# Kernel optimization log

Measured on AMD Instinct MI355X. Metric: run time of the kernel, lower is better.

The kernel has to match this reference:

```python
import jax, jax.numpy as jnp
import numpy as np

IOU_THRESHOLD = 0.5  # default in ObjectUtils.nms
N_BOXES = 10000


def setup_inputs() -> dict:
    key = jax.random.key(0)
    k1, k2 = jax.random.split(key)
    boxes = jax.random.uniform(k1, (N_BOXES, 4), dtype=jnp.float32)  # normalized cxcywh
    scores = jax.random.uniform(k2, (N_BOXES,), dtype=jnp.float32)
    return {"boxes_cxcywh": boxes, "scores": scores}


def _cxcywh_to_ltrb(b):
    cx, cy, w, h = b[:, 0], b[:, 1], b[:, 2], b[:, 3]
    return jnp.stack([cx - w / 2, cy - h / 2, cx + w / 2, cy + h / 2], axis=1)


def _pairwise_iou(a, b):
    # a: [N1,4] ltrb, b: [N2,4] ltrb -> [N1,N2] (matches ObjectUtils.compute_iou)
    lt = jnp.maximum(a[:, None, :2], b[None, :, :2])
    rb = jnp.minimum(a[:, None, 2:], b[None, :, 2:])
    wh = jnp.clip(rb - lt, 0.0)
    inter = wh[..., 0] * wh[..., 1]
    area_a = (a[:, 2] - a[:, 0]) * (a[:, 3] - a[:, 1])
    area_b = (b[:, 2] - b[:, 0]) * (b[:, 3] - b[:, 1])
    return inter / (area_a[:, None] + area_b[None, :] - inter)


def reference(boxes_cxcywh, scores):
    ltrb = _cxcywh_to_ltrb(boxes_cxcywh)
    iou = _pairwise_iou(ltrb, ltrb)  # [N,N]

    # ---- greedy NMS, faithful to ObjectUtils.nms (unclamped intersection,
    # retain when iou < threshold) expressed as a jit-friendly suppression loop ----
    n = ltrb.shape[0]
    order = jnp.argsort(-scores)  # highest score first (torch.sort ascending, pop last)
    bs = ltrb[order]
    l, t, r, b = bs[:, 0], bs[:, 1], bs[:, 2], bs[:, 3]
    area = (r - l) * (b - t)
    inter_nms = (jnp.minimum(r[:, None], r[None, :]) - jnp.maximum(l[:, None], l[None, :])) * \
                (jnp.minimum(b[:, None], b[None, :]) - jnp.maximum(t[:, None], t[None, :]))
    iou_nms = inter_nms / (area[:, None] + area[None, :] - inter_nms)
    ar = jnp.arange(n)

    def body(i, keep):
        # box i (in sorted order) suppresses lower-scored boxes only if it is itself kept
        suppress = keep[i] & (iou_nms[i] >= IOU_THRESHOLD) & (ar > i)
        return keep & jnp.logical_not(suppress)

    keep_sorted = jax.lax.fori_loop(0, n, body, jnp.ones((n,), dtype=bool))
    keep = jnp.zeros((n,), dtype=bool).at[order].set(keep_sorted)
    return iou, keep
```

## Files before the change

kernel.cpp:

```cpp
#include <hip/hip_runtime.h>

typedef unsigned long long u64;

#define THR 0.5f

__device__ __forceinline__ void conv_box(const float4 b, float& l, float& t,
                                         float& r, float& bo, float& a) {
  #pragma clang fp contract(off)
  float hw = 0.5f * b.z;
  float hh = 0.5f * b.w;
  l = b.x - hw;
  t = b.y - hh;
  r = b.x + hw;
  bo = b.y + hh;
  a = (r - l) * (bo - t);
}

__global__ void k_zero(int* __restrict__ rank, int n) {
  int i = blockIdx.x * blockDim.x + threadIdx.x;
  if (i < n) rank[i] = 0;
}

__global__ void k_rank(const float* __restrict__ scores, int* __restrict__ rank,
                       int n, int jchunk) {
  int i = blockIdx.x * blockDim.x + threadIdx.x;
  if (i >= n) return;
  float si = scores[i];
  int j0 = blockIdx.y * jchunk;
  int j1 = min(j0 + jchunk, n);
  int c = 0;
  for (int j = j0; j < j1; ++j) {
    float sj = scores[j];
    c += ((sj > si) || (sj == si && j < i)) ? 1 : 0;
  }
  if (c) atomicAdd(rank + i, c);
}

__global__ void k_scatter(const float4* __restrict__ boxes, const int* __restrict__ rank,
                          float* __restrict__ sl, float* __restrict__ st,
                          float* __restrict__ sr, float* __restrict__ sb,
                          float* __restrict__ sa, int* __restrict__ sidx, int n) {
  int i = blockIdx.x * blockDim.x + threadIdx.x;
  if (i >= n) return;
  float l, t, r, b, a;
  conv_box(boxes[i], l, t, r, b, a);
  int k = rank[i];
  sl[k] = l; st[k] = t; sr[k] = r; sb[k] = b; sa[k] = a; sidx[k] = i;
}

__device__ __forceinline__ void mask_body(
    const float* __restrict__ sl, const float* __restrict__ st,
    const float* __restrict__ sr, const float* __restrict__ sb,
    const float* __restrict__ sa,
    u64* __restrict__ mask, u64* __restrict__ diag, u64* __restrict__ band,
    int n, int wstride, int bx, int by) {
  #pragma clang fp contract(off)
  int k = bx * 256 + threadIdx.x;
  if (k >= n) return;
  int w = by;
  int jbase = w << 6;
  u64 word = 0;
  if (jbase + 63 > k) {
    float l = sl[k], t = st[k], r = sr[k], b = sb[k], a = sa[k];
    int jend = min(jbase + 64, n);
    for (int j = max(jbase, k + 1); j < jend; ++j) {
      float lmax = fmaxf(l, sl[j]);
      float tmax = fmaxf(t, st[j]);
      float rmin = fminf(r, sr[j]);
      float bmin = fminf(b, sb[j]);
      float wd = rmin - lmax;
      float hd = bmin - tmax;
      float inter = wd * hd;
      float denom = (a + sa[j]) - inter;
      float q = inter / denom;
      if (q >= THR) word |= 1ull << (j - jbase);
    }
  }
  mask[(size_t)k * wstride + w] = word;
  int kg = k >> 6;
  if (kg == w) diag[k] = word;
  if (w == kg + 1) band[k] = word;
}

__global__ void k_mask(const float* __restrict__ sl, const float* __restrict__ st,
                       const float* __restrict__ sr, const float* __restrict__ sb,
                       const float* __restrict__ sa,
                       u64* __restrict__ mask, u64* __restrict__ diag,
                       u64* __restrict__ band, int n, int wstride) {
  mask_body(sl, st, sr, sb, sa, mask, diag, band, n, wstride, blockIdx.x, blockIdx.y);
}

__device__ __forceinline__ u64 wave_or_u64(u64 v) {
  unsigned lo = (unsigned)v, hi = (unsigned)(v >> 32);
#define DPP_OR(x, ctrl, rmask) \
  x |= (unsigned)__builtin_amdgcn_update_dpp(0, (int)(x), ctrl, rmask, 0xF, true)
  DPP_OR(lo, 0x111, 0xF); DPP_OR(hi, 0x111, 0xF);
  DPP_OR(lo, 0x112, 0xF); DPP_OR(hi, 0x112, 0xF);
  DPP_OR(lo, 0x114, 0xF); DPP_OR(hi, 0x114, 0xF);
  DPP_OR(lo, 0x118, 0xF); DPP_OR(hi, 0x118, 0xF);
  DPP_OR(lo, 0x142, 0xA); DPP_OR(hi, 0x142, 0xA);
  DPP_OR(lo, 0x143, 0xC); DPP_OR(hi, 0x143, 0xC);
#undef DPP_OR
  unsigned flo = (unsigned)__builtin_amdgcn_readlane((int)lo, 63);
  unsigned fhi = (unsigned)__builtin_amdgcn_readlane((int)hi, 63);
  return ((u64)fhi << 32) | flo;
}

__device__ __forceinline__ void scan_body7(
    const u64* __restrict__ mask, const u64* __restrict__ diag,
    const u64* __restrict__ band, const int* __restrict__ sidx,
    float* __restrict__ keep, int n, int wstride,
    u64* rem, u64* dsh, u64* bsh, u64* kwords, int (*kept)[64], int* nk_sh) {
  int t = threadIdx.x, wv = t >> 6, lane = t & 63;
  int ng = (n + 63) >> 6;
  rem[t] = 0;
  if (t < 2) nk_sh[t] = 0;
  u64 bnd = 0;
  u64 x0 = 0, x1 = 0, x2 = 0, x3 = 0, x4 = 0, x5 = 0, x6 = 0, x7 = 0;
  const ulonglong2* d2 = (const ulonglong2*)dsh;
  if (wv == 0) {
    dsh[lane] = diag[lane];
    bsh[lane] = band[lane];
    ulonglong2 p0 = d2[0], p1 = d2[1], p2 = d2[2], p3 = d2[3];
    x0 = p0.x; x1 = p0.y; x2 = p1.x; x3 = p1.y;
    x4 = p2.x; x5 = p2.y; x6 = p3.x; x7 = p3.y;
  }
  __syncthreads();
  for (int g = 0; g < ng; ++g) {
    int base = g << 6;
    if (wv == 0) {
      int nxt = base + 64 + lane;
      u64 dnext = (g + 1 < ng) ? diag[nxt] : 0;
      u64 bnext = (g + 1 < ng) ? band[nxt] : 0;
      u64 bshv = bsh[lane];
      u64 s = rem[g] | bnd;
      int valid = n - base;
      if (valid < 64) s |= (~0ull) << valid;
      u64 kw = 0;
      u64 y0, y1, y2, y3, y4, y5, y6, y7;
#define LDC(a0,a1,a2,a3,a4,a5,a6,a7, c) { \
      ulonglong2 q0 = d2[4*(c)], q1 = d2[4*(c)+1], q2 = d2[4*(c)+2], q3 = d2[4*(c)+3]; \
      a0 = q0.x; a1 = q0.y; a2 = q1.x; a3 = q1.y; a4 = q2.x; a5 = q2.y; a6 = q3.x; a7 = q3.y; }
#define STEP(BB, EQ) if (!((s >> (BB)) & 1ull)) { kw |= 1ull << (BB); s |= EQ; }
#define CHUNK(b0v, a0,a1,a2,a3,a4,a5,a6,a7) \
      if ((unsigned)((s >> (b0v)) & 0xFFull) != 0xFFu) { \
        STEP(b0v+0, a0) STEP(b0v+1, a1) STEP(b0v+2, a2) STEP(b0v+3, a3) \
        STEP(b0v+4, a4) STEP(b0v+5, a5) STEP(b0v+6, a6) STEP(b0v+7, a7) }
      LDC(y0,y1,y2,y3,y4,y5,y6,y7, 1); CHUNK(0,  x0,x1,x2,x3,x4,x5,x6,x7);
      LDC(x0,x1,x2,x3,x4,x5,x6,x7, 2); CHUNK(8,  y0,y1,y2,y3,y4,y5,y6,y7);
      LDC(y0,y1,y2,y3,y4,y5,y6,y7, 3); CHUNK(16, x0,x1,x2,x3,x4,x5,x6,x7);
      LDC(x0,x1,x2,x3,x4,x5,x6,x7, 4); CHUNK(24, y0,y1,y2,y3,y4,y5,y6,y7);
      LDC(y0,y1,y2,y3,y4,y5,y6,y7, 5); CHUNK(32, x0,x1,x2,x3,x4,x5,x6,x7);
      LDC(x0,x1,x2,x3,x4,x5,x6,x7, 6); CHUNK(40, y0,y1,y2,y3,y4,y5,y6,y7);
      LDC(y0,y1,y2,y3,y4,y5,y6,y7, 7); CHUNK(48, x0,x1,x2,x3,x4,x5,x6,x7);
                                       CHUNK(56, y0,y1,y2,y3,y4,y5,y6,y7);
#undef CHUNK
#undef STEP
#undef LDC
      if (lane == 0) kwords[g] = kw;
      int nk = __popcll(kw);
      if ((kw >> lane) & 1ull) {
        int pos = __popcll(kw & ((1ull << lane) - 1ull));
        kept[g & 1][pos] = lane;
      }
      int npad = (nk + 15) & ~15;
      if (lane >= nk && lane < npad) kept[g & 1][lane] = 0;
      if (lane == 0) nk_sh[g & 1] = nk;
      u64 bv = ((kw >> lane) & 1ull) ? bshv : 0ull;
      bnd = wave_or_u64(bv);
      dsh[lane] = dnext;
      bsh[lane] = bnext;
      ulonglong2 p0 = d2[0], p1 = d2[1], p2 = d2[2], p3 = d2[3];
      x0 = p0.x; x1 = p0.y; x2 = p1.x; x3 = p1.y;
      x4 = p2.x; x5 = p2.y; x6 = p3.x; x7 = p3.y;
    } else {
      int w = t - 64;
      int gp = g - 1;
      if (gp >= 0 && w > g && w < ng) {
        int nkp = nk_sh[gp & 1];
        if (nkp) {
          const int* kp = kept[gp & 1];
          int basep = gp << 6;
          u64 acc = 0;
          for (int i = 0; i < nkp; i += 16) {
            int k0 = kp[i+0],  k1 = kp[i+1],  k2 = kp[i+2],  k3 = kp[i+3];
            int k4 = kp[i+4],  k5 = kp[i+5],  k6 = kp[i+6],  k7 = kp[i+7];
            int k8 = kp[i+8],  k9 = kp[i+9],  k10 = kp[i+10], k11 = kp[i+11];
            int k12 = kp[i+12], k13 = kp[i+13], k14 = kp[i+14], k15 = kp[i+15];
            u64 v0 = mask[(size_t)(basep + k0) * wstride + w];
            u64 v1 = mask[(size_t)(basep + k1) * wstride + w];
            u64 v2 = mask[(size_t)(basep + k2) * wstride + w];
            u64 v3 = mask[(size_t)(basep + k3) * wstride + w];
            u64 v4 = mask[(size_t)(basep + k4) * wstride + w];
            u64 v5 = mask[(size_t)(basep + k5) * wstride + w];
            u64 v6 = mask[(size_t)(basep + k6) * wstride + w];
            u64 v7 = mask[(size_t)(basep + k7) * wstride + w];
            u64 v8 = mask[(size_t)(basep + k8) * wstride + w];
            u64 v9 = mask[(size_t)(basep + k9) * wstride + w];
            u64 v10 = mask[(size_t)(basep + k10) * wstride + w];
            u64 v11 = mask[(size_t)(basep + k11) * wstride + w];
            u64 v12 = mask[(size_t)(basep + k12) * wstride + w];
            u64 v13 = mask[(size_t)(basep + k13) * wstride + w];
            u64 v14 = mask[(size_t)(basep + k14) * wstride + w];
            u64 v15 = mask[(size_t)(basep + k15) * wstride + w];
            acc |= v0;
            if (i + 1 < nkp)  acc |= v1;
            if (i + 2 < nkp)  acc |= v2;
            if (i + 3 < nkp)  acc |= v3;
            if (i + 4 < nkp)  acc |= v4;
            if (i + 5 < nkp)  acc |= v5;
            if (i + 6 < nkp)  acc |= v6;
            if (i + 7 < nkp)  acc |= v7;
            if (i + 8 < nkp)  acc |= v8;
            if (i + 9 < nkp)  acc |= v9;
            if (i + 10 < nkp) acc |= v10;
            if (i + 11 < nkp) acc |= v11;
            if (i + 12 < nkp) acc |= v12;
            if (i + 13 < nkp) acc |= v13;
            if (i + 14 < nkp) acc |= v14;
            if (i + 15 < nkp) acc |= v15;
          }
          rem[w] |= acc;
        }
      }
    }
    __syncthreads();
  }
  for (int k = t; k < n; k += 256) {
    u64 kwv = kwords[k >> 6];
    keep[sidx[k]] = ((kwv >> (k & 63)) & 1ull) ? 1.0f : 0.0f;
  }
}

__global__ __launch_bounds__(256, 1) void k_scan2(const u64* __restrict__ mask,
                                                  const u64* __restrict__ diag,
                                                  const u64* __restrict__ band,
                                                  const int* __restrict__ sidx,
                                                  float* __restrict__ keep,
                                                  int n, int wstride) {
  __shared__ u64 rem[256];
  __shared__ __align__(16) u64 dsh[64];
  __shared__ u64 bsh[64];
  __shared__ u64 kwords[160];
  __shared__ int kept[2][64];
  __shared__ int nk_sh[2];
  scan_body7(mask, diag, band, sidx, keep, n, wstride, rem, dsh, bsh, kwords, kept, nk_sh);
}

__device__ __forceinline__ float iou_one(float li, float ti, float ri, float bi, float ai,
                                         float lj, float tj, float rj, float bj, float aj) {
  float lmax = fmaxf(li, lj);
  float tmax = fmaxf(ti, tj);
  float rmin = fminf(ri, rj);
  float bmin = fminf(bi, bj);
  float w = fmaxf(rmin - lmax, 0.0f);
  float h = fmaxf(bmin - tmax, 0.0f);
  float inter = w * h;
  float denom = (ai + aj) - inter;
  return inter * __builtin_amdgcn_rcpf(denom);
}

__device__ __forceinline__ void iou_body(const float4* __restrict__ boxes,
                                         float* __restrict__ out,
                                         int n, int rpb, int bx, int by) {
  int nj4 = (n + 3) >> 2;
  int j4 = bx * 256 + threadIdx.x;
  if (j4 >= nj4) return;
  int j = j4 << 2;
  int jc1 = min(j + 1, n - 1), jc2 = min(j + 2, n - 1), jc3 = min(j + 3, n - 1);
  float l0,t0,r0,b0,a0, l1,t1,r1,b1,a1, l2,t2,r2,b2,a2, l3,t3,r3,b3,a3;
  conv_box(boxes[j],   l0,t0,r0,b0,a0);
  conv_box(boxes[jc1], l1,t1,r1,b1,a1);
  conv_box(boxes[jc2], l2,t2,r2,b2,a2);
  conv_box(boxes[jc3], l3,t3,r3,b3,a3);
  bool full = (j + 3) < n;
  for (int rr = 0; rr < rpb; ++rr) {
    int i = by * rpb + rr;
    if (i >= n) return;
    float li,ti,ri,bi,ai;
    conv_box(boxes[i], li,ti,ri,bi,ai);
    float4 o;
    o.x = iou_one(li,ti,ri,bi,ai, l0,t0,r0,b0,a0);
    o.y = iou_one(li,ti,ri,bi,ai, l1,t1,r1,b1,a1);
    o.z = iou_one(li,ti,ri,bi,ai, l2,t2,r2,b2,a2);
    o.w = iou_one(li,ti,ri,bi,ai, l3,t3,r3,b3,a3);
    size_t row = (size_t)i * n;
    if (full) {
      *reinterpret_cast<float4*>(out + row + j) = o;
    } else {
      out[row + j] = o.x;
      if (j + 1 < n) out[row + j + 1] = o.y;
      if (j + 2 < n) out[row + j + 2] = o.z;
    }
  }
}

__global__ void k_iou(const float4* __restrict__ boxes, float* __restrict__ out,
                      int n, int rpb) {
  iou_body(boxes, out, n, rpb, blockIdx.x, blockIdx.y);
}

__global__ __launch_bounds__(256) void k_maskiou(
    const float* __restrict__ sl, const float* __restrict__ st,
    const float* __restrict__ sr, const float* __restrict__ sb,
    const float* __restrict__ sa,
    u64* __restrict__ mask, u64* __restrict__ diag, u64* __restrict__ band,
    int wstride, const float4* __restrict__ boxes, float* __restrict__ out,
    int n, int rpb, int nbx, int nmask, int gx) {
  int id = blockIdx.x;
  if (id < nmask) {
    mask_body(sl, st, sr, sb, sa, mask, diag, band, n, wstride,
              id % nbx, id / nbx);
  } else {
    int iid = id - nmask;
    iou_body(boxes, out, n, rpb, iid % gx, iid / gx);
  }
}

extern "C" void kernel_launch(void* const* d_in, const int* in_sizes, int n_in,
                              void* d_out, int out_size, void* d_ws, size_t ws_size,
                              hipStream_t stream) {
  const float* boxes = (const float*)d_in[0];
  const float* scores = (const float*)d_in[1];
  int n = in_sizes[1];
  float* out = (float*)d_out;
  size_t NN = (size_t)n * (size_t)n;
  float* keep = out + NN;

  int words = (n + 63) >> 6;
  int wstride = (words + 3) & ~3;
  size_t need = (size_t)n * wstride * 8
              + (size_t)words * 64 * 8 * 2
              + 256
              + (size_t)n * 4 * 7;
  bool use_ws = (ws_size >= need);

  char* base = use_ws ? (char*)d_ws : (char*)d_out;
  size_t off = 0;
  u64* mask = (u64*)(base + off); off += (size_t)n * wstride * 8;
  u64* diag = (u64*)(base + off); off += (size_t)words * 64 * 8;
  u64* band = (u64*)(base + off); off += (size_t)words * 64 * 8;
  off = (off + 255) & ~(size_t)255;
  float* sl  = (float*)(base + off); off += (size_t)n * 4;
  float* st_ = (float*)(base + off); off += (size_t)n * 4;
  float* sr  = (float*)(base + off); off += (size_t)n * 4;
  float* sb  = (float*)(base + off); off += (size_t)n * 4;
  float* sa  = (float*)(base + off); off += (size_t)n * 4;
  int* sidx  = (int*)(base + off); off += (size_t)n * 4;
  int* rank  = (int*)(base + off); off += (size_t)n * 4;

  int nb = (n + 255) / 256;
  k_zero<<<nb, 256, 0, stream>>>(rank, n);

  int jblocks = 40;
  int jchunk = (n + jblocks - 1) / jblocks;
  k_rank<<<dim3(nb, jblocks), 256, 0, stream>>>(scores, rank, n, jchunk);

  k_scatter<<<nb, 256, 0, stream>>>((const float4*)boxes, rank, sl, st_, sr, sb, sa, sidx, n);

  int rpb = 10;
  int nj4 = (n + 3) >> 2;
  int gx = (nj4 + 255) / 256;
  int gy = (n + rpb - 1) / rpb;

  if (use_ws) {
    int nmask = nb * words;
    int total = nmask + gx * gy;
    k_maskiou<<<total, 256, 0, stream>>>(sl, st_, sr, sb, sa, mask, diag, band,
                                         wstride, (const float4*)boxes, out,
                                         n, rpb, nb, nmask, gx);
    k_scan2<<<1, 256, 0, stream>>>(mask, diag, band, sidx, keep, n, wstride);
  } else {
    k_mask<<<dim3(nb, words), 256, 0, stream>>>(sl, st_, sr, sb, sa, mask, diag, band, n, wstride);
    k_scan2<<<1, 256, 0, stream>>>(mask, diag, band, sidx, keep, n, wstride);
    k_iou<<<dim3(gx, gy), 256, 0, stream>>>((const float4*)boxes, out, n, rpb);
  }
}
```

Baseline: 409.0 us.

## Deepen NMS scan pipeline to two groups of lookahead with second band

The single-block greedy scan now precomputes two band words (next and next-next group) so the helper waves can lag two groups behind the serial wave. This gives the global mask gathers an extra iteration of latency hiding, using a triple-buffered kept list. The gather loop is unrolled to 32 loads, empty groups skip the wave reductions, and the IoU output uses nontemporal stores. The cost is extra band storage and writes, more registers, and modulo-3 indexing.

Result: slower. 460.6 us (+12.6%).

```diff
diff --git a/kernel.cpp b/kernel.cpp
--- a/kernel.cpp
+++ b/kernel.cpp
@@ -1,6 +1,7 @@
 #include <hip/hip_runtime.h>
 
 typedef unsigned long long u64;
+typedef float f32x4 __attribute__((ext_vector_type(4)));
 
 #define THR 0.5f
 
@@ -52,7 +53,8 @@
     const float* __restrict__ sl, const float* __restrict__ st,
     const float* __restrict__ sr, const float* __restrict__ sb,
     const float* __restrict__ sa,
-    u64* __restrict__ mask, u64* __restrict__ diag, u64* __restrict__ band,
+    u64* __restrict__ mask, u64* __restrict__ diag,
+    u64* __restrict__ band1, u64* __restrict__ band2,
     int n, int wstride, int bx, int by) {
   #pragma clang fp contract(off)
   int k = bx * 256 + threadIdx.x;
@@ -79,15 +81,18 @@
   mask[(size_t)k * wstride + w] = word;
   int kg = k >> 6;
   if (kg == w) diag[k] = word;
-  if (w == kg + 1) band[k] = word;
+  if (w == kg + 1) band1[k] = word;
+  if (w == kg + 2) band2[k] = word;
 }
 
 __global__ void k_mask(const float* __restrict__ sl, const float* __restrict__ st,
                        const float* __restrict__ sr, const float* __restrict__ sb,
                        const float* __restrict__ sa,
                        u64* __restrict__ mask, u64* __restrict__ diag,
-                       u64* __restrict__ band, int n, int wstride) {
-  mask_body(sl, st, sr, sb, sa, mask, diag, band, n, wstride, blockIdx.x, blockIdx.y);
+                       u64* __restrict__ band1, u64* __restrict__ band2,
+                       int n, int wstride) {
+  mask_body(sl, st, sr, sb, sa, mask, diag, band1, band2, n, wstride,
+            blockIdx.x, blockIdx.y);
 }
 
 __device__ __forceinline__ u64 wave_or_u64(u64 v) {
@@ -106,21 +111,24 @@
   return ((u64)fhi << 32) | flo;
 }
 
-__device__ __forceinline__ void scan_body7(
+__device__ __forceinline__ void scan_body8(
     const u64* __restrict__ mask, const u64* __restrict__ diag,
-    const u64* __restrict__ band, const int* __restrict__ sidx,
-    float* __restrict__ keep, int n, int wstride,
-    u64* rem, u64* dsh, u64* bsh, u64* kwords, int (*kept)[64], int* nk_sh) {
+    const u64* __restrict__ band1, const u64* __restrict__ band2,
+    const int* __restrict__ sidx, float* __restrict__ keep,
+    int n, int wstride,
+    u64* rem, u64* dsh, u64* bsh1, u64* bsh2, u64* kwords,
+    int (*kept)[64], int* nk_sh) {
   int t = threadIdx.x, wv = t >> 6, lane = t & 63;
   int ng = (n + 63) >> 6;
   rem[t] = 0;
-  if (t < 2) nk_sh[t] = 0;
-  u64 bnd = 0;
+  if (t < 3) nk_sh[t] = 0;
+  u64 R1 = 0, R2 = 0;
   u64 x0 = 0, x1 = 0, x2 = 0, x3 = 0, x4 = 0, x5 = 0, x6 = 0, x7 = 0;
   const ulonglong2* d2 = (const ulonglong2*)dsh;
   if (wv == 0) {
     dsh[lane] = diag[lane];
-    bsh[lane] = band[lane];
+    bsh1[lane] = band1[lane];
+    bsh2[lane] = band2[lane];
     ulonglong2 p0 = d2[0], p1 = d2[1], p2 = d2[2], p3 = d2[3];
     x0 = p0.x; x1 = p0.y; x2 = p1.x; x3 = p1.y;
     x4 = p2.x; x5 = p2.y; x6 = p3.x; x7 = p3.y;
@@ -130,10 +138,12 @@
     int base = g << 6;
     if (wv == 0) {
       int nxt = base + 64 + lane;
-      u64 dnext = (g + 1 < ng) ? diag[nxt] : 0;
-      u64 bnext = (g + 1 < ng) ? band[nxt] : 0;
-      u64 bshv = bsh[lane];
-      u64 s = rem[g] | bnd;
+      bool hn = (g + 1 < ng);
+      u64 dnext = hn ? diag[nxt] : 0;
+      u64 b1next = hn ? band1[nxt] : 0;
+      u64 b2next = hn ? band2[nxt] : 0;
+      u64 b1v = bsh1[lane], b2v = bsh2[lane];
+      u64 s = rem[g] | R1;
       int valid = n - base;
       if (valid < 64) s |= (~0ull) << valid;
       u64 kw = 0;
@@ -158,67 +168,52 @@
 #undef STEP
 #undef LDC
       if (lane == 0) kwords[g] = kw;
-      int nk = __popcll(kw);
-      if ((kw >> lane) & 1ull) {
-        int pos = __popcll(kw & ((1ull << lane) - 1ull));
-        kept[g & 1][pos] = lane;
+      u64 c1 = 0, c2 = 0;
+      if (kw) {
+        int nk = __popcll(kw);
+        if ((kw >> lane) & 1ull) {
+          int pos = __popcll(kw & ((1ull << lane) - 1ull));
+          kept[g % 3][pos] = lane;
+        }
+        int npad = (nk + 31) & ~31;
+        if (lane >= nk && lane < npad) kept[g % 3][lane] = 0;
+        if (lane == 0) nk_sh[g % 3] = nk;
+        u64 m = (u64)0 - ((kw >> lane) & 1ull);
+        c1 = wave_or_u64(b1v & m);
+        c2 = wave_or_u64(b2v & m);
+      } else {
+        if (lane == 0) nk_sh[g % 3] = 0;
       }
-      int npad = (nk + 15) & ~15;
-      if (lane >= nk && lane < npad) kept[g & 1][lane] = 0;
-      if (lane == 0) nk_sh[g & 1] = nk;
-      u64 bv = ((kw >> lane) & 1ull) ? bshv : 0ull;
-      bnd = wave_or_u64(bv);
+      R1 = R2 | c1;
+      R2 = c2;
       dsh[lane] = dnext;
-      bsh[lane] = bnext;
+      bsh1[lane] = b1next;
+      bsh2[lane] = b2next;
       ulonglong2 p0 = d2[0], p1 = d2[1], p2 = d2[2], p3 = d2[3];
       x0 = p0.x; x1 = p0.y; x2 = p1.x; x3 = p1.y;
       x4 = p2.x; x5 = p2.y; x6 = p3.x; x7 = p3.y;
     } else {
       int w = t - 64;
-      int gp = g - 1;
+      int gp = g - 2;
       if (gp >= 0 && w > g && w < ng) {
-        int nkp = nk_sh[gp & 1];
+        int nkp = nk_sh[gp % 3];
         if (nkp) {
-          const int* kp = kept[gp & 1];
+          const int* kp = kept[gp % 3];
           int basep = gp << 6;
           u64 acc = 0;
-          for (int i = 0; i < nkp; i += 16) {
-            int k0 = kp[i+0],  k1 = kp[i+1],  k2 = kp[i+2],  k3 = kp[i+3];
-            int k4 = kp[i+4],  k5 = kp[i+5],  k6 = kp[i+6],  k7 = kp[i+7];
-            int k8 = kp[i+8],  k9 = kp[i+9],  k10 = kp[i+10], k11 = kp[i+11];
-            int k12 = kp[i+12], k13 = kp[i+13], k14 = kp[i+14], k15 = kp[i+15];
-            u64 v0 = mask[(size_t)(basep + k0) * wstride + w];
-            u64 v1 = mask[(size_t)(basep + k1) * wstride + w];
-            u64 v2 = mask[(size_t)(basep + k2) * wstride + w];
-            u64 v3 = mask[(size_t)(basep + k3) * wstride + w];
-            u64 v4 = mask[(size_t)(basep + k4) * wstride + w];
-            u64 v5 = mask[(size_t)(basep + k5) * wstride + w];
-            u64 v6 = mask[(size_t)(basep + k6) * wstride + w];
-            u64 v7 = mask[(size_t)(basep + k7) * wstride + w];
-            u64 v8 = mask[(size_t)(basep + k8) * wstride + w];
-            u64 v9 = mask[(size_t)(basep + k9) * wstride + w];
-            u64 v10 = mask[(size_t)(basep + k10) * wstride + w];
-            u64 v11 = mask[(size_t)(basep + k11) * wstride + w];
-            u64 v12 = mask[(size_t)(basep + k12) * wstride + w];
-            u64 v13 = mask[(size_t)(basep + k13) * wstride + w];
-            u64 v14 = mask[(size_t)(basep + k14) * wstride + w];
-            u64 v15 = mask[(size_t)(basep + k15) * wstride + w];
-            acc |= v0;
-            if (i + 1 < nkp)  acc |= v1;
-            if (i + 2 < nkp)  acc |= v2;
-            if (i + 3 < nkp)  acc |= v3;
-            if (i + 4 < nkp)  acc |= v4;
-            if (i + 5 < nkp)  acc |= v5;
-            if (i + 6 < nkp)  acc |= v6;
-            if (i + 7 < nkp)  acc |= v7;
-            if (i + 8 < nkp)  acc |= v8;
-            if (i + 9 < nkp)  acc |= v9;
-            if (i + 10 < nkp) acc |= v10;
-            if (i + 11 < nkp) acc |= v11;
-            if (i + 12 < nkp) acc |= v12;
-            if (i + 13 < nkp) acc |= v13;
-            if (i + 14 < nkp) acc |= v14;
-            if (i + 15 < nkp) acc |= v15;
+          for (int i = 0; i < nkp; i += 32) {
+#define LD1(q) u64 v##q = mask[(size_t)(basep + kp[i + q]) * wstride + w];
+            LD1(0)  LD1(1)  LD1(2)  LD1(3)  LD1(4)  LD1(5)  LD1(6)  LD1(7)
+            LD1(8)  LD1(9)  LD1(10) LD1(11) LD1(12) LD1(13) LD1(14) LD1(15)
+            LD1(16) LD1(17) LD1(18) LD1(19) LD1(20) LD1(21) LD1(22) LD1(23)
+            LD1(24) LD1(25) LD1(26) LD1(27) LD1(28) LD1(29) LD1(30) LD1(31)
+#undef LD1
+#define ACC(q) if (i + q < nkp) acc |= v##q;
+            ACC(0)  ACC(1)  ACC(2)  ACC(3)  ACC(4)  ACC(5)  ACC(6)  ACC(7)
+            ACC(8)  ACC(9)  ACC(10) ACC(11) ACC(12) ACC(13) ACC(14) ACC(15)
+            ACC(16) ACC(17) ACC(18) ACC(19) ACC(20) ACC(21) ACC(22) ACC(23)
+            ACC(24) ACC(25) ACC(26) ACC(27) ACC(28) ACC(29) ACC(30) ACC(31)
+#undef ACC
           }
           rem[w] |= acc;
         }
@@ -234,17 +229,20 @@
 
 __global__ __launch_bounds__(256, 1) void k_scan2(const u64* __restrict__ mask,
                                                   const u64* __restrict__ diag,
-                                                  const u64* __restrict__ band,
+                                                  const u64* __restrict__ band1,
+                                                  const u64* __restrict__ band2,
                                                   const int* __restrict__ sidx,
                                                   float* __restrict__ keep,
                                                   int n, int wstride) {
   __shared__ u64 rem[256];
   __shared__ __align__(16) u64 dsh[64];
-  __shared__ u64 bsh[64];
+  __shared__ u64 bsh1[64];
+  __shared__ u64 bsh2[64];
   __shared__ u64 kwords[160];
-  __shared__ int kept[2][64];
-  __shared__ int nk_sh[2];
-  scan_body7(mask, diag, band, sidx, keep, n, wstride, rem, dsh, bsh, kwords, kept, nk_sh);
+  __shared__ int kept[3][64];
+  __shared__ int nk_sh[3];
+  scan_body8(mask, diag, band1, band2, sidx, keep, n, wstride,
+             rem, dsh, bsh1, bsh2, kwords, kept, nk_sh);
 }
 
 __device__ __forceinline__ float iou_one(float li, float ti, float ri, float bi, float ai,
@@ -286,7 +284,8 @@
     o.w = iou_one(li,ti,ri,bi,ai, l3,t3,r3,b3,a3);
     size_t row = (size_t)i * n;
     if (full) {
-      *reinterpret_cast<float4*>(out + row + j) = o;
+      f32x4 ov = { o.x, o.y, o.z, o.w };
+      __builtin_nontemporal_store(ov, reinterpret_cast<f32x4*>(out + row + j));
     } else {
       out[row + j] = o.x;
       if (j + 1 < n) out[row + j + 1] = o.y;
@@ -304,12 +303,13 @@
     const float* __restrict__ sl, const float* __restrict__ st,
     const float* __restrict__ sr, const float* __restrict__ sb,
     const float* __restrict__ sa,
-    u64* __restrict__ mask, u64* __restrict__ diag, u64* __restrict__ band,
+    u64* __restrict__ mask, u64* __restrict__ diag,
+    u64* __restrict__ band1, u64* __restrict__ band2,
     int wstride, const float4* __restrict__ boxes, float* __restrict__ out,
     int n, int rpb, int nbx, int nmask, int gx) {
   int id = blockIdx.x;
   if (id < nmask) {
-    mask_body(sl, st, sr, sb, sa, mask, diag, band, n, wstride,
+    mask_body(sl, st, sr, sb, sa, mask, diag, band1, band2, n, wstride,
               id % nbx, id / nbx);
   } else {
     int iid = id - nmask;
@@ -330,16 +330,17 @@
   int words = (n + 63) >> 6;
   int wstride = (words + 3) & ~3;
   size_t need = (size_t)n * wstride * 8
-              + (size_t)words * 64 * 8 * 2
+              + (size_t)words * 64 * 8 * 3
               + 256
               + (size_t)n * 4 * 7;
   bool use_ws = (ws_size >= need);
 
   char* base = use_ws ? (char*)d_ws : (char*)d_out;
   size_t off = 0;
-  u64* mask = (u64*)(base + off); off += (size_t)n * wstride * 8;
-  u64* diag = (u64*)(base + off); off += (size_t)words * 64 * 8;
-  u64* band = (u64*)(base + off); off += (size_t)words * 64 * 8;
+  u64* mask  = (u64*)(base + off); off += (size_t)n * wstride * 8;
+  u64* diag  = (u64*)(base + off); off += (size_t)words * 64 * 8;
+  u64* band1 = (u64*)(base + off); off += (size_t)words * 64 * 8;
+  u64* band2 = (u64*)(base + off); off += (size_t)words * 64 * 8;
   off = (off + 255) & ~(size_t)255;
   float* sl  = (float*)(base + off); off += (size_t)n * 4;
   float* st_ = (float*)(base + off); off += (size_t)n * 4;
@@ -366,13 +367,14 @@
   if (use_ws) {
     int nmask = nb * words;
     int total = nmask + gx * gy;
-    k_maskiou<<<total, 256, 0, stream>>>(sl, st_, sr, sb, sa, mask, diag, band,
-                                         wstride, (const float4*)boxes, out,
-                                         n, rpb, nb, nmask, gx);
-    k_scan2<<<1, 256, 0, stream>>>(mask, diag, band, sidx, keep, n, wstride);
+    k_maskiou<<<total, 256, 0, stream>>>(sl, st_, sr, sb, sa, mask, diag, band1,
+                                         band2, wstride, (const float4*)boxes,
+                                         out, n, rpb, nb, nmask, gx);
+    k_scan2<<<1, 256, 0, stream>>>(mask, diag, band1, band2, sidx, keep, n, wstride);
   } else {
-    k_mask<<<dim3(nb, words), 256, 0, stream>>>(sl, st_, sr, sb, sa, mask, diag, band, n, wstride);
-    k_scan2<<<1, 256, 0, stream>>>(mask, diag, band, sidx, keep, n, wstride);
+    k_mask<<<dim3(nb, words), 256, 0, stream>>>(sl, st_, sr, sb, sa, mask, diag,
+                                                band1, band2, n, wstride);
+    k_scan2<<<1, 256, 0, stream>>>(mask, diag, band1, band2, sidx, keep, n, wstride);
     k_iou<<<dim3(gx, gy), 256, 0, stream>>>((const float4*)boxes, out, n, rpb);
   }
 }
```
